# Kernel tuning notes

Hardware: AMD Instinct MI355X
Metric: run time of the kernel (lower is better)

## Reference

```python
import jax, jax.numpy as jnp
import numpy as np

B, S, D, E, H, TOPK = 4, 1024, 512, 8, 1536, 2
NORM_EPS = 1e-5

def _ln(x, w, b, eps=1e-5):
    m = jnp.mean(x, -1, keepdims=True)
    v = jnp.var(x, -1, keepdims=True)  # biased var, as torch LayerNorm
    return (x - m) * jax.lax.rsqrt(v + eps) * w + b

def _modulate(x, shift, scale):
    return x * (1 + scale[:, None, :]) + shift[:, None, :]

def setup_inputs() -> dict:
    key = jax.random.key(0)
    ks = jax.random.split(key, 14)
    s = 0.02
    return dict(
        x=jax.random.normal(ks[0], (B, S, D), jnp.float32),
        c=jax.random.normal(ks[1], (B, D), jnp.float32),
        W_ada=jax.random.normal(ks[2], (D, 6 * D), jnp.float32) * s,
        b_ada=jax.random.normal(ks[3], (6 * D,), jnp.float32) * 0.1,
        Wq=jax.random.normal(ks[4], (D, D), jnp.float32) * s,
        Wk=jax.random.normal(ks[5], (D, D), jnp.float32) * s,
        Wv=jax.random.normal(ks[6], (D, D), jnp.float32) * s,
        Wo=jax.random.normal(ks[7], (D, D), jnp.float32) * s,
        qn_w=jnp.ones((D,), jnp.float32), qn_b=jnp.zeros((D,), jnp.float32),
        kn_w=jnp.ones((D,), jnp.float32), kn_b=jnp.zeros((D,), jnp.float32),
        an_w=jnp.ones((D,), jnp.float32), an_b=jnp.zeros((D,), jnp.float32),
        fn_w=jnp.ones((D,), jnp.float32), fn_b=jnp.zeros((D,), jnp.float32),
        Wr=jax.random.normal(ks[8], (D, E), jnp.float32) * s,
        br=jnp.zeros((E,), jnp.float32),
        W1=jax.random.normal(ks[9], (E, D, H), jnp.float32) * s,
        W2=jax.random.normal(ks[10], (E, H, D), jnp.float32) * s,
        W3=jax.random.normal(ks[11], (E, D, H), jnp.float32) * s,
    )

def reference(x, c, W_ada, b_ada, Wq, Wk, Wv, Wo, qn_w, qn_b, kn_w, kn_b,
              an_w, an_b, fn_w, fn_b, Wr, br, W1, W2, W3):
    # adaLN conditioning: SiLU -> Linear -> 6 chunks
    mods = jax.nn.silu(c) @ W_ada + b_ada          # (B, 6D)
    sh_msa, sc_msa, g_msa, sh_mlp, sc_mlp, g_mlp = jnp.split(mods, 6, axis=1)

    # Attention (source attends over the FEATURE dim: scores are (B, D, D))
    h = _modulate(_ln(x, an_w, an_b, NORM_EPS), sh_msa, sc_msa)
    q = _ln(h @ Wq, qn_w, qn_b)
    k = _ln(h @ Wk, kn_w, kn_b)
    v = h @ Wv
    scores = jnp.einsum('bsd,bse->bde', q, k)      # (B, D, D), no 1/sqrt scale (as source)
    A = jax.nn.softmax(scores, axis=-1)
    attn = jnp.einsum('bde,bse->bsd', A, v) @ Wo   # (B, S, D)
    x = x + g_msa[:, None, :] * attn

    # MoE feed-forward (top-2 routing; output REPLACES x, no residual/gate per source)
    xm = _modulate(_ln(x, fn_w, fn_b, NORM_EPS), sh_mlp, sc_mlp)
    logits = xm @ Wr + br                          # (B, S, E)
    # F.normalize default dim=1 -> L2 normalize over the SEQUENCE axis (faithful)
    nrm = jnp.sqrt(jnp.sum(logits * logits, axis=1, keepdims=True))
    logits = logits / jnp.maximum(nrm, 1e-12)
    probs = jax.nn.softmax(logits, axis=-1)        # (B, S, E)
    vals, idx = jax.lax.top_k(probs, TOPK)

    T = B * S
    xf = xm.reshape(T, D)
    # dense combine weights: zero for unselected experts (same math as gather/scatter-add)
    wden = jnp.zeros((T, E), xf.dtype).at[jnp.arange(T)[:, None], idx.reshape(T, TOPK)].set(vals.reshape(T, TOPK))
    h1 = jnp.einsum('td,edh->teh', xf, W1)
    h3 = jnp.einsum('td,edh->teh', xf, W3)
    y = jnp.einsum('teh,ehd->ted', jnp.sin(h1) * h3, W2)  # sin-gated FFN per expert
    moe = jnp.einsum('ted,te->td', y, wden).reshape(B, S, D)

    avg = probs.mean(axis=0)                       # mean over batch dim only (faithful): (S, E)
    aux = jnp.sum((1.0 / E - avg) ** 2)
    return moe, aux
```

## Files before the change

kernel.cpp:

```cpp
#include <hip/hip_runtime.h>
#include <math.h>

#define NB 4
#define NS 1024
#define ND 512
#define NE 8
#define NH 1536
#define NT 4096
#define D6 3072

typedef _Float16 half_t;
typedef _Float16 f16x8 __attribute__((ext_vector_type(8)));
typedef _Float16 f16x4 __attribute__((ext_vector_type(4)));
typedef float    f32x4 __attribute__((ext_vector_type(4)));

#define LDC 136
#define TM_MAX 71

__device__ __forceinline__ void gld16(const void* g, void* l) {
  __builtin_amdgcn_global_load_lds((const __attribute__((address_space(1))) char*)g,
                                   (__attribute__((address_space(3))) char*)l, 16, 0, 0);
}

__device__ __forceinline__ int xcd_chunk(int bid, int nwg) {
  int xcd = bid & 7, ixc = bid >> 3;
  int q = nwg >> 3, r = nwg & 7;
  return (xcd < r ? xcd * (q + 1) : r * (q + 1) + (xcd - r) * q) + ixc;
}

__device__ __forceinline__ int resolve_tile(const int* __restrict__ offs, int t,
                                            int& e_out, int& m0_out) {
  int acc = 0, found = 0, ee = 0, mm = 0;
  #pragma unroll
  for (int q = 0; q < NE; ++q) {
    int ne_q = offs[q + 1] - offs[q];
    int te = (ne_q + 127) >> 7;
    if (!found && t < acc + te) { ee = q; mm = (t - acc) << 7; found = 1; }
    acc += te;
  }
  e_out = ee; m0_out = mm;
  return found;
}

__global__ __launch_bounds__(256) void k_ada(const float* __restrict__ c,
    const float* __restrict__ Wada, const float* __restrict__ bada,
    float* __restrict__ mods)
{
  __shared__ float sc[ND];
  __shared__ float part[256];
  int tid = threadIdx.x;
  int blk = blockIdx.x;
  int o0 = blk * 64;
  int b = o0 / D6;
  int j0 = o0 - b * D6;
  for (int d = tid; d < ND; d += 256) {
    float v = c[b * ND + d];
    sc[d] = v / (1.f + expf(-v));
  }
  __syncthreads();
  int j = j0 + (tid & 63);
  int kc = tid >> 6;
  float acc = 0.f;
  #pragma unroll 8
  for (int d = kc * 128; d < kc * 128 + 128; ++d)
    acc += sc[d] * Wada[(size_t)d * D6 + j];
  part[tid] = acc;
  __syncthreads();
  if (tid < 64) {
    float r = part[tid] + part[tid + 64] + part[tid + 128] + part[tid + 192]
            + bada[j0 + tid];
    mods[b * D6 + j0 + tid] = r;
  }
}

__global__ __launch_bounds__(256) void k_lnmod(const float* X, int xstride,
    float* Yf, half_t* Yh, half_t* Yl, int ystride,
    const float* __restrict__ w, const float* __restrict__ b,
    const float* __restrict__ mods, int sh_off, int sc_off,
    const float* __restrict__ Wr, const float* __restrict__ br,
    float* __restrict__ logits)
{
  __shared__ float red[16];
  __shared__ float red2[32];
  int tid = threadIdx.x;
  int row = blockIdx.x;
  int batch = row >> 10;
  const float* xr = X + (size_t)row * xstride;
  float x0 = xr[tid], x1 = xr[tid + 256];
  float s = x0 + x1, q = x0 * x0 + x1 * x1;
  #pragma unroll
  for (int off = 32; off > 0; off >>= 1) { s += __shfl_down(s, off, 64); q += __shfl_down(q, off, 64); }
  if ((tid & 63) == 0) { red[tid >> 6] = s; red[8 + (tid >> 6)] = q; }
  __syncthreads();
  if (tid == 0) {
    float S = red[0] + red[1] + red[2] + red[3];
    float Q = red[8] + red[9] + red[10] + red[11];
    float mean = S * (1.f / (float)ND);
    float var = Q * (1.f / (float)ND) - mean * mean;
    red[0] = mean; red[1] = rsqrtf(var + 1e-5f);
  }
  __syncthreads();
  float mean = red[0], rstd = red[1];
  int d0 = tid, d1 = tid + 256;
  float y0 = (x0 - mean) * rstd * w[d0] + b[d0];
  float y1 = (x1 - mean) * rstd * w[d1] + b[d1];
  if (mods) {
    const float* mb = mods + batch * D6;
    y0 = y0 * (1.f + mb[sc_off + d0]) + mb[sh_off + d0];
    y1 = y1 * (1.f + mb[sc_off + d1]) + mb[sh_off + d1];
  }
  size_t o0 = (size_t)row * ystride + d0, o1 = (size_t)row * ystride + d1;
  if (Yf) { Yf[o0] = y0; Yf[o1] = y1; }
  if (Yh) {
    half_t h0 = (half_t)y0, h1 = (half_t)y1;
    Yh[o0] = h0; Yh[o1] = h1;
    if (Yl) { Yl[o0] = (half_t)(y0 - (float)h0); Yl[o1] = (half_t)(y1 - (float)h1); }
  }
  if (Wr) {
    float p[8];
    float4 wa = *(const float4*)(Wr + d0 * 8);
    float4 wb = *(const float4*)(Wr + d0 * 8 + 4);
    float4 wc = *(const float4*)(Wr + d1 * 8);
    float4 wd = *(const float4*)(Wr + d1 * 8 + 4);
    p[0] = y0 * wa.x + y1 * wc.x; p[1] = y0 * wa.y + y1 * wc.y;
    p[2] = y0 * wa.z + y1 * wc.z; p[3] = y0 * wa.w + y1 * wc.w;
    p[4] = y0 * wb.x + y1 * wd.x; p[5] = y0 * wb.y + y1 * wd.y;
    p[6] = y0 * wb.z + y1 * wd.z; p[7] = y0 * wb.w + y1 * wd.w;
    #pragma unroll
    for (int off = 32; off > 0; off >>= 1)
      #pragma unroll
      for (int e = 0; e < 8; ++e) p[e] += __shfl_down(p[e], off, 64);
    if ((tid & 63) == 0) {
      #pragma unroll
      for (int e = 0; e < 8; ++e) red2[(tid >> 6) * 8 + e] = p[e];
    }
    __syncthreads();
    if (tid < 8)
      logits[(size_t)row * 8 + tid] = red2[tid] + red2[8 + tid] + red2[16 + tid]
                                    + red2[24 + tid] + br[tid];
  }
}

__global__ __launch_bounds__(256) void k_lnqk(float* QKV,
    const float* __restrict__ qw, const float* __restrict__ qb,
    const float* __restrict__ kw, const float* __restrict__ kb)
{
  __shared__ float red[16];
  int tid = threadIdx.x;
  int row = blockIdx.x >> 1;
  int h = blockIdx.x & 1;
  const float* w = h ? kw : qw;
  const float* b = h ? kb : qb;
  float* xr = QKV + (size_t)row * 1536 + h * 512;
  float x0 = xr[tid], x1 = xr[tid + 256];
  float s = x0 + x1, q = x0 * x0 + x1 * x1;
  #pragma unroll
  for (int off = 32; off > 0; off >>= 1) { s += __shfl_down(s, off, 64); q += __shfl_down(q, off, 64); }
  if ((tid & 63) == 0) { red[tid >> 6] = s; red[8 + (tid >> 6)] = q; }
  __syncthreads();
  if (tid == 0) {
    float S = red[0] + red[1] + red[2] + red[3];
    float Q = red[8] + red[9] + red[10] + red[11];
    float mean = S * (1.f / (float)ND);
    float var = Q * (1.f / (float)ND) - mean * mean;
    red[0] = mean; red[1] = rsqrtf(var + 1e-5f);
  }
  __syncthreads();
  float mean = red[0], rstd = red[1];
  xr[tid]       = (x0 - mean) * rstd * w[tid] + b[tid];
  xr[tid + 256] = (x1 - mean) * rstd * w[tid + 256] + b[tid + 256];
}

__global__ __launch_bounds__(256) void k_tsplit2(const float* __restrict__ QKV,
    half_t* __restrict__ H0, half_t* __restrict__ L0)
{
  __shared__ float tile[32][33];
  int z = blockIdx.z;
  half_t* outH = H0 + (size_t)z * 4194304;
  half_t* outL = L0 + (size_t)z * 4194304;
  int col0 = z * 512;
  int s0 = blockIdx.x * 32, c0 = blockIdx.y * 32;
  int tid = threadIdx.x;
  int r = tid >> 5, c = tid & 31;
  #pragma unroll
  for (int p = 0; p < 4; ++p)
    tile[r + p * 8][c] = QKV[(size_t)(s0 + r + p * 8) * 1536 + col0 + c0 + c];
  __syncthreads();
  #pragma unroll
  for (int p = 0; p < 4; ++p) {
    float v = tile[c][r + p * 8];
    half_t h = (half_t)v;
    size_t o = (size_t)(c0 + r + p * 8) * NT + s0 + c;
    outH[o] = h; outL[o] = (half_t)(v - (float)h);
  }
}

__global__ __launch_bounds__(256) void k_wsplit4(const float* __restrict__ Wq,
    const float* __restrict__ Wk, const float* __restrict__ Wv,
    const float* __restrict__ Wo, half_t* __restrict__ outH, half_t* __restrict__ outL)
{
  __shared__ float tile[32][33];
  int z = blockIdx.z;
  const float* W = (z == 0) ? Wq : (z == 1) ? Wk : (z == 2) ? Wv : Wo;
  int rowoff = z * 512;
  int k0 = blockIdx.x * 32, n0 = blockIdx.y * 32;
  int tid = threadIdx.x;
  int r = tid >> 5, c = tid & 31;
  #pragma unroll
  for (int p = 0; p < 4; ++p)
    tile[r + p * 8][c] = W[(size_t)(k0 + r + p * 8) * ND + n0 + c];
  __syncthreads();
  #pragma unroll
  for (int p = 0; p < 4; ++p) {
    float v = tile[c][r + p * 8];
    half_t h = (half_t)v;
    size_t o = (size_t)(rowoff + n0 + r + p * 8) * ND + k0 + c;
    outH[o] = h; outL[o] = (half_t)(v - (float)h);
  }
}

__global__ __launch_bounds__(256) void k_vsplit(const float* __restrict__ QKV,
    half_t* __restrict__ Vh, half_t* __restrict__ Vl)
{
  int i = blockIdx.x * 256 + threadIdx.x;
  int s = i >> 7, c = (i & 127) * 4;
  float4 v = *(const float4*)(QKV + (size_t)s * 1536 + 1024 + c);
  f16x4 h, l;
  h[0] = (half_t)v.x; l[0] = (half_t)(v.x - (float)h[0]);
  h[1] = (half_t)v.y; l[1] = (half_t)(v.y - (float)h[1]);
  h[2] = (half_t)v.z; l[2] = (half_t)(v.z - (float)h[2]);
  h[3] = (half_t)v.w; l[3] = (half_t)(v.w - (float)h[3]);
  *(f16x4*)(Vh + (size_t)s * ND + c) = h;
  *(f16x4*)(Vl + (size_t)s * ND + c) = l;
}

template<int MODE>
__global__ __launch_bounds__(256, 2) void k_gemm_hl(
    const half_t* __restrict__ Ah, const half_t* __restrict__ Al, long long sAz,
    const half_t* __restrict__ Bh, const half_t* __restrict__ Bl, long long sBz,
    int lda, int ldb, int K,
    float* __restrict__ Cf, half_t* __restrict__ Ch, half_t* __restrict__ Cl,
    long long sCz, int ldc,
    const float* __restrict__ xres, const float* __restrict__ mods)
{
  int z = blockIdx.z;
  int m0 = blockIdx.x * 128, n0 = blockIdx.y * 128;
  __shared__ __align__(16) char smem[65536];
  half_t* Sh = (half_t*)smem;
  int tid = threadIdx.x;
  int lane = tid & 63, w = tid >> 6;
  int wm = (w >> 1) * 64, wn = (w & 1) * 64;
  int qd = lane >> 4, md = lane & 15;
  int rA0 = tid >> 2;
  int sw = (((tid & 3) ^ ((tid >> 3) & 3)) << 3);

  const half_t* pAh0 = Ah + z * sAz + (size_t)(m0 + rA0) * lda + sw;
  const half_t* pAh1 = pAh0 + (size_t)64 * lda;
  const half_t* pAl0 = Al + z * sAz + (size_t)(m0 + rA0) * lda + sw;
  const half_t* pAl1 = pAl0 + (size_t)64 * lda;
  const half_t* pBh0 = Bh + z * sBz + (size_t)(n0 + rA0) * ldb + sw;
  const half_t* pBh1 = pBh0 + (size_t)64 * ldb;
  const half_t* pBl0 = Bl + z * sBz + (size_t)(n0 + rA0) * ldb + sw;
  const half_t* pBl1 = pBl0 + (size_t)64 * ldb;

  char* dAh = smem + w * 1024;
  char* dAl = smem + 16384 + w * 1024;
  char* dBh = smem + 32768 + w * 1024;
  char* dBl = smem + 49152 + w * 1024;

  f32x4 acc[4][4];
  #pragma unroll
  for (int i = 0; i < 4; ++i)
    #pragma unroll
    for (int j = 0; j < 4; ++j)
      #pragma unroll
      for (int p = 0; p < 4; ++p) acc[i][j][p] = 0.f;

  int swq  = ((qd ^ ((md >> 1) & 3)) << 3);
  int aoff = (wm + md) * 32 + swq;
  int boff = (wn + md) * 32 + swq;

#define GEMM_STAGE(p, kk) do { int kb_ = (kk); int pb_ = (p) * 8192;         \
    gld16(pAh0 + kb_, dAh + pb_); gld16(pAh1 + kb_, dAh + pb_ + 4096);       \
    gld16(pAl0 + kb_, dAl + pb_); gld16(pAl1 + kb_, dAl + pb_ + 4096);       \
    gld16(pBh0 + kb_, dBh + pb_); gld16(pBh1 + kb_, dBh + pb_ + 4096);       \
    gld16(pBl0 + kb_, dBl + pb_); gld16(pBl1 + kb_, dBl + pb_ + 4096); } while (0)

  int iters = K >> 5;
  GEMM_STAGE(0, 0);
  int cur = 0;
  #pragma unroll 1
  for (int it = 0; it < iters; ++it) {
    if (it + 1 < iters) {
      GEMM_STAGE(cur ^ 1, (it + 1) * 32);
      asm volatile("s_waitcnt vmcnt(8)\ns_barrier" ::: "memory");
    } else {
      asm volatile("s_waitcnt vmcnt(0)\ns_barrier" ::: "memory");
    }
    const half_t* Ash = Sh + cur * 4096;
    const half_t* Asl = Sh + 8192  + cur * 4096;
    const half_t* Bsh = Sh + 16384 + cur * 4096;
    const half_t* Bsl = Sh + 24576 + cur * 4096;
    f16x8 ah[4], al[4], bh[4], bl[4];
    #pragma unroll
    for (int i = 0; i < 4; ++i) {
      ah[i] = *(const f16x8*)(Ash + aoff + i * 512);
      al[i] = *(const f16x8*)(Asl + aoff + i * 512);
    }
    #pragma unroll
    for (int j = 0; j < 4; ++j) {
      bh[j] = *(const f16x8*)(Bsh + boff + j * 512);
      bl[j] = *(const f16x8*)(Bsl + boff + j * 512);
    }
    __builtin_amdgcn_s_setprio(1);
    #pragma unroll
    for (int i = 0; i < 4; ++i)
      #pragma unroll
      for (int j = 0; j < 4; ++j) {
        acc[i][j] = __builtin_amdgcn_mfma_f32_16x16x32_f16(ah[i], bh[j], acc[i][j], 0, 0, 0);
        acc[i][j] = __builtin_amdgcn_mfma_f32_16x16x32_f16(ah[i], bl[j], acc[i][j], 0, 0, 0);
        acc[i][j] = __builtin_amdgcn_mfma_f32_16x16x32_f16(al[i], bh[j], acc[i][j], 0, 0, 0);
      }
    __builtin_amdgcn_s_setprio(0);
    asm volatile("s_barrier" ::: "memory");
    cur ^= 1;
  }
#undef GEMM_STAGE

  if (MODE == 1) {
    half_t* Cs = (half_t*)smem;
    __syncthreads();
    #pragma unroll
    for (int i = 0; i < 4; ++i)
      #pragma unroll
      for (int j = 0; j < 4; ++j)
        #pragma unroll
        for (int p = 0; p < 4; ++p)
          Cs[(wm + 16 * i + qd * 4 + p) * LDC + wn + 16 * j + md] = (half_t)acc[i][j][p];
    __syncthreads();
    #pragma unroll
    for (int it2 = 0; it2 < 8; ++it2) {
      int chunk = it2 * 256 + tid;
      int r = chunk >> 4, c8 = (chunk & 15) * 8;
      *(f16x8*)(Ch + z * sCz + (size_t)(m0 + r) * ldc + n0 + c8) = *(const f16x8*)(Cs + r * LDC + c8);
    }
    __syncthreads();
    #pragma unroll
    for (int i = 0; i < 4; ++i)
      #pragma unroll
      for (int j = 0; j < 4; ++j)
        #pragma unroll
        for (int p = 0; p < 4; ++p) {
          float v = acc[i][j][p];
          half_t h = (half_t)v;
          Cs[(wm + 16 * i + qd * 4 + p) * LDC + wn + 16 * j + md] = (half_t)(v - (float)h);
        }
    __syncthreads();
    #pragma unroll
    for (int it2 = 0; it2 < 8; ++it2) {
      int chunk = it2 * 256 + tid;
      int r = chunk >> 4, c8 = (chunk & 15) * 8;
      *(f16x8*)(Cl + z * sCz + (size_t)(m0 + r) * ldc + n0 + c8) = *(const f16x8*)(Cs + r * LDC + c8);
    }
  } else {
    #pragma unroll
    for (int i = 0; i < 4; ++i)
      #pragma unroll
      for (int p = 0; p < 4; ++p) {
        int r = m0 + wm + 16 * i + qd * 4 + p;
        float* cp = Cf + z * sCz + (size_t)r * ldc + n0 + wn + md;
        if (MODE == 2) {
          int batch = r >> 10;
          const float* mb = mods + batch * D6 + 2 * ND;
          const float* xp = xres + (size_t)r * ldc + n0 + wn + md;
          #pragma unroll
          for (int j = 0; j < 4; ++j) {
            int col = wn + md + 16 * j;
            cp[16 * j] = xp[16 * j] + mb[n0 + col] * acc[i][j][p];
          }
        } else {
          #pragma unroll
          for (int j = 0; j < 4; ++j) cp[16 * j] = acc[i][j][p];
        }
      }
  }
}

__global__ __launch_bounds__(256) void k_softmax512_sum4(const float* __restrict__ SC4,
    half_t* __restrict__ Ph, half_t* __restrict__ Pl)
{
  __shared__ float red[16];
  int tid = threadIdx.x;
  int row = blockIdx.x;
  int b = row >> 9, d = row & 511;
  const float* r0 = SC4 + ((size_t)(b * 4 + 0) << 18) + (size_t)d * ND;
  const float* r1 = SC4 + ((size_t)(b * 4 + 1) << 18) + (size_t)d * ND;
  const float* r2 = SC4 + ((size_t)(b * 4 + 2) << 18) + (size_t)d * ND;
  const float* r3 = SC4 + ((size_t)(b * 4 + 3) << 18) + (size_t)d * ND;
  float x0 = r0[tid] + r1[tid] + r2[tid] + r3[tid];
  float x1 = r0[tid + 256] + r1[tid + 256] + r2[tid + 256] + r3[tid + 256];
  float m = fmaxf(x0, x1);
  #pragma unroll
  for (int off = 32; off > 0; off >>= 1) m = fmaxf(m, __shfl_down(m, off, 64));
  if ((tid & 63) == 0) red[tid >> 6] = m;
  __syncthreads();
  if (tid == 0) red[0] = fmaxf(fmaxf(red[0], red[1]), fmaxf(red[2], red[3]));
  __syncthreads();
  m = red[0];
  float e0 = expf(x0 - m), e1 = expf(x1 - m);
  float s = e0 + e1;
  #pragma unroll
  for (int off = 32; off > 0; off >>= 1) s += __shfl_down(s, off, 64);
  if ((tid & 63) == 0) red[8 + (tid >> 6)] = s;
  __syncthreads();
  if (tid == 0) red[8] = red[8] + red[9] + red[10] + red[11];
  __syncthreads();
  float inv = 1.f / red[8];
  float p0 = e0 * inv, p1 = e1 * inv;
  size_t base = (size_t)row * ND;
  half_t h0 = (half_t)p0, h1 = (half_t)p1;
  Ph[base + tid] = h0;       Pl[base + tid] = (half_t)(p0 - (float)h0);
  Ph[base + tid + 256] = h1; Pl[base + tid + 256] = (half_t)(p1 - (float)h1);
}

__global__ __launch_bounds__(256) void k_colnorm(const float* __restrict__ logits,
    float* __restrict__ nrm)
{
  __shared__ float red[8];
  int tid = threadIdx.x;
  int b = blockIdx.x >> 3, e = blockIdx.x & 7;
  float acc = 0.f;
  for (int s = tid; s < NS; s += 256) {
    float l = logits[((size_t)(b << 10) + s) * NE + e];
    acc += l * l;
  }
  #pragma unroll
  for (int off = 32; off > 0; off >>= 1) acc += __shfl_down(acc, off, 64);
  if ((tid & 63) == 0) red[tid >> 6] = acc;
  __syncthreads();
  if (tid == 0) nrm[b * NE + e] = sqrtf(red[0] + red[1] + red[2] + red[3]);
}

__global__ __launch_bounds__(1024) void k_route(const float* __restrict__ logits,
    const float* __restrict__ nrm, float* __restrict__ probs,
    float* __restrict__ wsel, int* __restrict__ offs_g,
    int* __restrict__ list, int* __restrict__ inv)
{
  __shared__ unsigned char sisel[8192];
  __shared__ int cw[8][16][8];
  __shared__ int soffs[9];
  __shared__ float snrm[32];
  int tid = threadIdx.x;
  int lane = tid & 63, wv = tid >> 6;
  if (tid < 32) snrm[tid] = fmaxf(nrm[tid], 1e-12f);
  __syncthreads();
  #pragma unroll 1
  for (int c = 0; c < 4; ++c) {
    int t = c * 1024 + tid;
    int b = t >> 10;
    float p[8];
    float4 l0 = *(const float4*)(logits + (size_t)t * 8);
    float4 l1 = *(const float4*)(logits + (size_t)t * 8 + 4);
    p[0] = l0.x / snrm[b * 8 + 0]; p[1] = l0.y / snrm[b * 8 + 1];
    p[2] = l0.z / snrm[b * 8 + 2]; p[3] = l0.w / snrm[b * 8 + 3];
    p[4] = l1.x / snrm[b * 8 + 4]; p[5] = l1.y / snrm[b * 8 + 5];
    p[6] = l1.z / snrm[b * 8 + 6]; p[7] = l1.w / snrm[b * 8 + 7];
    float mx = p[0];
    #pragma unroll
    for (int e = 1; e < 8; ++e) mx = fmaxf(mx, p[e]);
    float s = 0.f;
    #pragma unroll
    for (int e = 0; e < 8; ++e) { p[e] = expf(p[e] - mx); s += p[e]; }
    float invs = 1.f / s;
    #pragma unroll
    for (int e = 0; e < 8; ++e) { p[e] *= invs; probs[(size_t)t * 8 + e] = p[e]; }
    int i1 = 0;
    #pragma unroll
    for (int e = 1; e < 8; ++e) if (p[e] > p[i1]) i1 = e;
    int i2 = (i1 == 0) ? 1 : 0;
    #pragma unroll
    for (int e = 0; e < 8; ++e) if (e != i1 && p[e] > p[i2]) i2 = e;
    wsel[t * 2] = p[i1]; wsel[t * 2 + 1] = p[i2];
    sisel[t * 2] = (unsigned char)i1; sisel[t * 2 + 1] = (unsigned char)i2;
  }
  __syncthreads();
  #pragma unroll 1
  for (int c = 0; c < 8; ++c) {
    int em = sisel[c * 1024 + tid];
    #pragma unroll
    for (int e = 0; e < 8; ++e) {
      unsigned long long mask = __ballot(em == e);
      if (lane == 0) cw[c][wv][e] = (int)__popcll(mask);
    }
  }
  __syncthreads();
  if (tid < 8) {
    int e = tid, run = 0;
    for (int c = 0; c < 8; ++c)
      for (int w2 = 0; w2 < 16; ++w2) { int v = cw[c][w2][e]; cw[c][w2][e] = run; run += v; }
    soffs[e] = run;
  }
  __syncthreads();
  if (tid == 0) {
    int a = 0;
    #pragma unroll
    for (int e = 0; e < 8; ++e) { int v = soffs[e]; soffs[e] = a; a += v; }
    soffs[8] = a;
  }
  __syncthreads();
  if (tid < 9) offs_g[tid] = soffs[tid];
  #pragma unroll 1
  for (int c = 0; c < 8; ++c) {
    int idx = c * 1024 + tid;
    int em = sisel[idx];
    int rk = 0;
    #pragma unroll
    for (int e = 0; e < 8; ++e) {
      unsigned long long mask = __ballot(em == e);
      if (em == e) rk = (int)__popcll(mask & ((1ull << lane) - 1ull));
    }
    int slot = soffs[em] + cw[c][wv][em] + rk;
    list[slot] = idx >> 1;
    inv[idx] = slot;
  }
}

__global__ __launch_bounds__(256) void k_aux(const float* __restrict__ probs,
    float* __restrict__ outAux)
{
  __shared__ float red[8];
  int tid = threadIdx.x;
  float acc = 0.f;
  for (int s = tid; s < NS; s += 256) {
    #pragma unroll
    for (int e = 0; e < NE; ++e) {
      float a = probs[(size_t)s * NE + e] + probs[(size_t)(NS + s) * NE + e]
              + probs[(size_t)(2 * NS + s) * NE + e] + probs[(size_t)(3 * NS + s) * NE + e];
      float d = 0.125f - a * 0.25f;
      acc += d * d;
    }
  }
  #pragma unroll
  for (int off = 32; off > 0; off >>= 1) acc += __shfl_down(acc, off, 64);
  if ((tid & 63) == 0) red[tid >> 6] = acc;
  __syncthreads();
  if (tid == 0) *outAux = red[0] + red[1] + red[2] + red[3];
}

__global__ __launch_bounds__(256) void k_tcast13(const float* __restrict__ W1,
    const float* __restrict__ W3, half_t* __restrict__ W1t, half_t* __restrict__ W3t)
{
  __shared__ float tile[32][33];
  int z = blockIdx.z;
  int sel = z >> 3, e = z & 7;
  const float* We = (sel ? W3 : W1) + (size_t)e * ND * NH;
  half_t* Wte = (sel ? W3t : W1t) + (size_t)e * ND * NH;
  int k0 = blockIdx.x * 32, n0 = blockIdx.y * 32;
  int tid = threadIdx.x;
  int r = tid >> 5, c = tid & 31;
  #pragma unroll
  for (int p = 0; p < 4; ++p)
    tile[r + p * 8][c] = We[(size_t)(k0 + r + p * 8) * NH + n0 + c];
  __syncthreads();
  #pragma unroll
  for (int p = 0; p < 4; ++p)
    Wte[(size_t)(n0 + r + p * 8) * ND + k0 + c] = (half_t)tile[c][r + p * 8];
}

__global__ __launch_bounds__(256) void k_tcastW2(const float* __restrict__ W,
    half_t* __restrict__ Wt)
{
  __shared__ float tile[32][33];
  const float* We = W + (size_t)blockIdx.z * NH * ND;
  half_t* Wte = Wt + (size_t)blockIdx.z * NH * ND;
  int k0 = blockIdx.x * 32, n0 = blockIdx.y * 32;
  int tid = threadIdx.x;
  int r = tid >> 5, c = tid & 31;
  #pragma unroll
  for (int p = 0; p < 4; ++p)
    tile[r + p * 8][c] = We[(size_t)(k0 + r + p * 8) * ND + n0 + c];
  __syncthreads();
  #pragma unroll
  for (int p = 0; p < 4; ++p)
    Wte[(size_t)(n0 + r + p * 8) * NH + k0 + c] = (half_t)tile[c][r + p * 8];
}

__global__ __launch_bounds__(256, 3) void k_ffn_fused(const half_t* __restrict__ xmh,
    const half_t* __restrict__ W1t, const half_t* __restrict__ W3t,
    const int* __restrict__ list, const int* __restrict__ offs,
    half_t* __restrict__ gate)
{
  int bx = xcd_chunk(blockIdx.x, TM_MAX * 12);
  int n0 = (bx % 12) * 128;
  int t  = bx / 12;
  int e, m0;
  if (!resolve_tile(offs, t, e, m0)) return;
  int base = offs[e], ne = offs[e + 1] - base;

  __shared__ __align__(16) char smem[49664];
  half_t* Sh = (half_t*)smem;
  int* rowt = (int*)(smem + 49152);
  int tid = threadIdx.x;
  if (tid < 128) {
    int rr = m0 + tid;
    rowt[tid] = (rr < ne) ? list[base + rr] : 0;
  }
  __syncthreads();

  int lane = tid & 63, w = tid >> 6;
  int wm = (w >> 1) * 64, wn = (w & 1) * 64;
  int qd = lane >> 4, md = lane & 15;
  int rA0 = tid >> 2;
  int sw = (((tid & 3) ^ ((tid >> 3) & 3)) << 3);
  int tok0 = rowt[rA0], tok1 = rowt[rA0 + 64];

  const half_t* gA0  = xmh + (size_t)tok0 * ND + sw;
  const half_t* gA1  = xmh + (size_t)tok1 * ND + sw;
  const half_t* gB10 = W1t + ((size_t)e * NH + n0 + rA0) * ND + sw;
  const half_t* gB11 = gB10 + (size_t)64 * ND;
  const half_t* gB30 = W3t + ((size_t)e * NH + n0 + rA0) * ND + sw;
  const half_t* gB31 = gB30 + (size_t)64 * ND;

  char* dA  = smem + w * 1024;
  char* dB1 = smem + 16384 + w * 1024;
  char* dB3 = smem + 32768 + w * 1024;

  f32x4 acc1[4][4], acc3[4][4];
  #pragma unroll
  for (int i = 0; i < 4; ++i)
    #pragma unroll
    for (int j = 0; j < 4; ++j)
      #pragma unroll
      for (int p = 0; p < 4; ++p) { acc1[i][j][p] = 0.f; acc3[i][j][p] = 0.f; }

  int swq  = ((qd ^ ((md >> 1) & 3)) << 3);
  int aoff = (wm + md) * 32 + swq;
  int boff = (wn + md) * 32 + swq;

#define FFN_STAGE(p, kk) do { int kb_ = (kk); int pb_ = (p) * 8192;          \
    gld16(gA0  + kb_, dA  + pb_); gld16(gA1  + kb_, dA  + pb_ + 4096);       \
    gld16(gB10 + kb_, dB1 + pb_); gld16(gB11 + kb_, dB1 + pb_ + 4096);       \
    gld16(gB30 + kb_, dB3 + pb_); gld16(gB31 + kb_, dB3 + pb_ + 4096); } while (0)

  FFN_STAGE(0, 0);
  int cur = 0;
  #pragma unroll 1
  for (int it = 0; it < 16; ++it) {
    if (it + 1 < 16) {
      FFN_STAGE(cur ^ 1, (it + 1) * 32);
      asm volatile("s_waitcnt vmcnt(6)\ns_barrier" ::: "memory");
    } else {
      asm volatile("s_waitcnt vmcnt(0)\ns_barrier" ::: "memory");
    }
    const half_t* As  = Sh + cur * 4096;
    const half_t* B1s = Sh + 8192  + cur * 4096;
    const half_t* B3s = Sh + 16384 + cur * 4096;
    f16x8 a[4];
    #pragma unroll
    for (int i = 0; i < 4; ++i) a[i] = *(const f16x8*)(As + aoff + i * 512);
    __builtin_amdgcn_s_setprio(1);
    #pragma unroll
    for (int j = 0; j < 4; ++j) {
      f16x8 b1 = *(const f16x8*)(B1s + boff + j * 512);
      f16x8 b3 = *(const f16x8*)(B3s + boff + j * 512);
      #pragma unroll
      for (int i = 0; i < 4; ++i) {
        acc1[i][j] = __builtin_amdgcn_mfma_f32_16x16x32_f16(a[i], b1, acc1[i][j], 0, 0, 0);
        acc3[i][j] = __builtin_amdgcn_mfma_f32_16x16x32_f16(a[i], b3, acc3[i][j], 0, 0, 0);
      }
    }
    __builtin_amdgcn_s_setprio(0);
    asm volatile("s_barrier" ::: "memory");
    cur ^= 1;
  }
#undef FFN_STAGE

  half_t* Cs = (half_t*)smem;
  #pragma unroll
  for (int i = 0; i < 4; ++i)
    #pragma unroll
    for (int j = 0; j < 4; ++j)
      #pragma unroll
      for (int p = 0; p < 4; ++p) {
        int rr = wm + 16 * i + qd * 4 + p;
        int cc = wn + 16 * j + md;
        Cs[rr * LDC + cc] = (half_t)(__sinf(acc1[i][j][p]) * acc3[i][j][p]);
      }
  __syncthreads();
  #pragma unroll
  for (int it = 0; it < 8; ++it) {
    int chunk = it * 256 + tid;
    int rr = chunk >> 4, c8 = (chunk & 15) * 8;
    if (m0 + rr < ne) {
      *(f16x8*)(gate + (size_t)(base + m0 + rr) * NH + n0 + c8) = *(const f16x8*)(Cs + rr * LDC + c8);
    }
  }
}

__global__ __launch_bounds__(256, 4) void k_moe2_mfma(const half_t* __restrict__ gate,
    const half_t* __restrict__ W2t, const int* __restrict__ offs,
    float* __restrict__ P)
{
  int bx = xcd_chunk(blockIdx.x, TM_MAX * 4);
  int n0 = (bx & 3) * 128;
  int t = bx >> 2;
  int e, m0;
  if (!resolve_tile(offs, t, e, m0)) return;
  int base = offs[e], ne = offs[e + 1] - base;

  __shared__ __align__(16) char smem[32768];
  half_t* Sh = (half_t*)smem;
  int tid = threadIdx.x;
  int lane = tid & 63, w = tid >> 6;
  int wm = (w >> 1) * 64, wn = (w & 1) * 64;
  int qd = lane >> 4, md = lane & 15;
  int rA0 = tid >> 2;
  int sw = (((tid & 3) ^ ((tid >> 3) & 3)) << 3);

  int ar0 = m0 + rA0;      if (ar0 >= ne) ar0 = ne - 1;
  int ar1 = m0 + rA0 + 64; if (ar1 >= ne) ar1 = ne - 1;
  const half_t* gA0 = gate + (size_t)(base + ar0) * NH + sw;
  const half_t* gA1 = gate + (size_t)(base + ar1) * NH + sw;
  const half_t* gB0 = W2t + ((size_t)e * ND + n0 + rA0) * NH + sw;
  const half_t* gB1 = gB0 + (size_t)64 * NH;

  char* dA = smem + w * 1024;
  char* dB = smem + 16384 + w * 1024;

  f32x4 acc[4][4];
  #pragma unroll
  for (int i = 0; i < 4; ++i)
    #pragma unroll
    for (int j = 0; j < 4; ++j)
      #pragma unroll
      for (int p = 0; p < 4; ++p) acc[i][j][p] = 0.f;

  int swq  = ((qd ^ ((md >> 1) & 3)) << 3);
  int aoff = (wm + md) * 32 + swq;
  int boff = (wn + md) * 32 + swq;

#define MOE2_STAGE(p, kk) do { int kb_ = (kk); int pb_ = (p) * 8192;         \
    gld16(gA0 + kb_, dA + pb_); gld16(gA1 + kb_, dA + pb_ + 4096);           \
    gld16(gB0 + kb_, dB + pb_); gld16(gB1 + kb_, dB + pb_ + 4096); } while (0)

  MOE2_STAGE(0, 0);
  int cur = 0;
  #pragma unroll 1
  for (int it = 0; it < 48; ++it) {
    if (it + 1 < 48) {
      MOE2_STAGE(cur ^ 1, (it + 1) * 32);
      asm volatile("s_waitcnt vmcnt(4)\ns_barrier" ::: "memory");
    } else {
      asm volatile("s_waitcnt vmcnt(0)\ns_barrier" ::: "memory");
    }
    const half_t* As = Sh + cur * 4096;
    const half_t* Bs = Sh + 8192 + cur * 4096;
    f16x8 a[4], b[4];
    #pragma unroll
    for (int i = 0; i < 4; ++i) a[i] = *(const f16x8*)(As + aoff + i * 512);
    #pragma unroll
    for (int j = 0; j < 4; ++j) b[j] = *(const f16x8*)(Bs + boff + j * 512);
    __builtin_amdgcn_s_setprio(1);
    #pragma unroll
    for (int j = 0; j < 4; ++j)
      #pragma unroll
      for (int i = 0; i < 4; ++i)
        acc[i][j] = __builtin_amdgcn_mfma_f32_16x16x32_f16(a[i], b[j], acc[i][j], 0, 0, 0);
    __builtin_amdgcn_s_setprio(0);
    asm volatile("s_barrier" ::: "memory");
    cur ^= 1;
  }
#undef MOE2_STAGE

  #pragma unroll
  for (int i = 0; i < 4; ++i)
    #pragma unroll
    for (int p = 0; p < 4; ++p) {
      int gr = m0 + wm + 16 * i + qd * 4 + p;
      if (gr < ne) {
        float* pp = P + (size_t)(base + gr) * ND + n0 + wn + md;
        #pragma unroll
        for (int j = 0; j < 4; ++j)
          pp[16 * j] = acc[i][j][p];
      }
    }
}

__global__ __launch_bounds__(256) void k_moe_reduce(const float* __restrict__ P,
    const int* __restrict__ inv, const float* __restrict__ wsel,
    float* __restrict__ out)
{
  int i = blockIdx.x * 256 + threadIdx.x;
  int t = i >> 7, d4 = i & 127;
  int s1 = inv[t * 2], s2 = inv[t * 2 + 1];
  float w1 = wsel[t * 2], w2 = wsel[t * 2 + 1];
  const float4* P4 = (const float4*)P;
  float4 a = P4[(size_t)s1 * 128 + d4];
  float4 b = P4[(size_t)s2 * 128 + d4];
  float4 o;
  o.x = w1 * a.x + w2 * b.x;
  o.y = w1 * a.y + w2 * b.y;
  o.z = w1 * a.z + w2 * b.z;
  o.w = w1 * a.w + w2 * b.w;
  ((float4*)out)[i] = o;
}

static const size_t BO_MODS  = 0;
static const size_t BO_HH    = 65536;
static const size_t BO_HL2   = 4259840;
static const size_t BO_PH    = 4259840;
static const size_t BO_PL    = 6357056;
static const size_t BO_WALLH = 8454144;
static const size_t BO_WALLL = 10551296;
static const size_t BO_QKV   = 12648448;
static const size_t BO_A0H   = 12648448;
static const size_t BO_A0L   = 16842752;
static const size_t BO_SC4   = 21037056;
static const size_t BO_X2    = 21037056;
static const size_t BO_XM    = 29425664;
static const size_t BO_QTH   = 37814272;
static const size_t BO_QTL   = 42008576;
static const size_t BO_KTH   = 46202880;
static const size_t BO_KTL   = 50397184;
static const size_t BO_VH    = 54591488;
static const size_t BO_VL    = 58785792;
static const size_t BO_W1T   = 37814272;
static const size_t BO_XMH   = 50397184;
static const size_t BO_W3T   = 65536;
static const size_t BO_GATE  = 12648448;
static const size_t BO_W2T   = 65536;
static const size_t BO_P     = 37814272;
static const size_t BO_LOGI  = 62980096;
static const size_t BO_NRM   = 63111168;
static const size_t BO_PROB  = 63111296;
static const size_t BO_WSEL  = 63242368;
static const size_t BO_INTS  = 63307904;

extern "C" void kernel_launch(void* const* d_in, const int* in_sizes, int n_in,
                              void* d_out, int out_size, void* d_ws, size_t ws_size,
                              hipStream_t stream)
{
  const float* x    = (const float*)d_in[0];
  const float* c    = (const float*)d_in[1];
  const float* Wada = (const float*)d_in[2];
  const float* bada = (const float*)d_in[3];
  const float* Wq   = (const float*)d_in[4];
  const float* Wk   = (const float*)d_in[5];
  const float* Wv   = (const float*)d_in[6];
  const float* Wo   = (const float*)d_in[7];
  const float* qn_w = (const float*)d_in[8];
  const float* qn_b = (const float*)d_in[9];
  const float* kn_w = (const float*)d_in[10];
  const float* kn_b = (const float*)d_in[11];
  const float* an_w = (const float*)d_in[12];
  const float* an_b = (const float*)d_in[13];
  const float* fn_w = (const float*)d_in[14];
  const float* fn_b = (const float*)d_in[15];
  const float* Wr   = (const float*)d_in[16];
  const float* br   = (const float*)d_in[17];
  const float* W1   = (const float*)d_in[18];
  const float* W2   = (const float*)d_in[19];
  const float* W3   = (const float*)d_in[20];
  float* out = (float*)d_out;
  char*  ws8 = (char*)d_ws;
  float* MODS = (float*)(ws8 + BO_MODS);
  half_t* Hh = (half_t*)(ws8 + BO_HH),   *Hl = (half_t*)(ws8 + BO_HL2);
  half_t* Ph = (half_t*)(ws8 + BO_PH),   *Pl = (half_t*)(ws8 + BO_PL);
  half_t* WALLH = (half_t*)(ws8 + BO_WALLH), *WALLL = (half_t*)(ws8 + BO_WALLL);
  half_t* WoTh = WALLH + (size_t)1536 * ND,  *WoTl = WALLL + (size_t)1536 * ND;
  float* QKV = (float*)(ws8 + BO_QKV);
  half_t* A0h = (half_t*)(ws8 + BO_A0H), *A0l = (half_t*)(ws8 + BO_A0L);
  float* SC4 = (float*)(ws8 + BO_SC4);
  float* X2  = (float*)(ws8 + BO_X2);
  float* XM  = (float*)(ws8 + BO_XM);
  half_t* qTh = (half_t*)(ws8 + BO_QTH), *qTl = (half_t*)(ws8 + BO_QTL);
  half_t* kTh = (half_t*)(ws8 + BO_KTH), *kTl = (half_t*)(ws8 + BO_KTL);
  half_t* Vh  = (half_t*)(ws8 + BO_VH),  *Vl  = (half_t*)(ws8 + BO_VL);
  half_t* W1T = (half_t*)(ws8 + BO_W1T);
  half_t* W3T = (half_t*)(ws8 + BO_W3T);
  half_t* W2T = (half_t*)(ws8 + BO_W2T);
  half_t* XMH = (half_t*)(ws8 + BO_XMH);
  half_t* GATEH = (half_t*)(ws8 + BO_GATE);
  float* PBUF = (float*)(ws8 + BO_P);
  float* LOGI = (float*)(ws8 + BO_LOGI);
  float* NRM  = (float*)(ws8 + BO_NRM);
  float* PROB = (float*)(ws8 + BO_PROB);
  float* WSEL = (float*)(ws8 + BO_WSEL);
  int* ib   = (int*)(ws8 + BO_INTS);
  int* offs = ib + 8208;
  int* list = ib + 8224;
  int* inv  = ib + 16416;

  k_ada<<<192, 256, 0, stream>>>(c, Wada, bada, MODS);
  k_wsplit4<<<dim3(16, 16, 4), 256, 0, stream>>>(Wq, Wk, Wv, Wo, WALLH, WALLL);
  k_lnmod<<<NT, 256, 0, stream>>>(x, ND, nullptr, Hh, Hl, ND, an_w, an_b, MODS, 0, 512,
                                  nullptr, nullptr, nullptr);
  k_gemm_hl<0><<<dim3(32, 12, 1), 256, 0, stream>>>(Hh, Hl, 0, WALLH, WALLL, 0,
      ND, ND, ND, QKV, nullptr, nullptr, 0, 1536, nullptr, nullptr);
  k_lnqk<<<2 * NT, 256, 0, stream>>>(QKV, qn_w, qn_b, kn_w, kn_b);
  k_tsplit2<<<dim3(128, 16, 2), 256, 0, stream>>>(QKV, qTh, qTl);
  k_vsplit<<<2048, 256, 0, stream>>>(QKV, Vh, Vl);
  k_gemm_hl<0><<<dim3(4, 4, 16), 256, 0, stream>>>(qTh, qTl, 256, kTh, kTl, 256,
      NT, NT, 256, SC4, nullptr, nullptr, 262144, ND, nullptr, nullptr);
  k_softmax512_sum4<<<2048, 256, 0, stream>>>(SC4, Ph, Pl);
  k_gemm_hl<1><<<dim3(8, 4, 4), 256, 0, stream>>>(Vh, Vl, 524288, Ph, Pl, 262144,
      ND, ND, ND, nullptr, A0h, A0l, 524288, ND, nullptr, nullptr);
  k_gemm_hl<2><<<dim3(32, 4, 1), 256, 0, stream>>>(A0h, A0l, 0, WoTh, WoTl, 0,
      ND, ND, ND, X2, nullptr, nullptr, 0, ND, x, MODS);
  k_lnmod<<<NT, 256, 0, stream>>>(X2, ND, XM, XMH, nullptr, ND, fn_w, fn_b, MODS, 1536, 2048,
                                  Wr, br, LOGI);
  k_colnorm<<<32, 256, 0, stream>>>(LOGI, NRM);
  k_route<<<1, 1024, 0, stream>>>(LOGI, NRM, PROB, WSEL, offs, list, inv);
  k_aux<<<1, 256, 0, stream>>>(PROB, out + (size_t)NT * ND);
  k_tcast13<<<dim3(16, 48, 16), 256, 0, stream>>>(W1, W3, W1T, W3T);
  k_ffn_fused<<<TM_MAX * 12, 256, 0, stream>>>(XMH, W1T, W3T, list, offs, GATEH);
  k_tcastW2<<<dim3(48, 16, 8), 256, 0, stream>>>(W2, W2T);
  k_moe2_mfma<<<TM_MAX * 4, 256, 0, stream>>>(GATEH, W2T, offs, PBUF);
  k_moe_reduce<<<2048, 256, 0, stream>>>(PBUF, inv, WSEL, out);
}
```

Before: 396.3 us.

## Fuse V hi/lo split into QKV GEMM epilogue and widen weight transposes

Adds a GEMM epilogue mode that writes the V columns of the QKV projection straight out as fp16 hi/lo pairs, which removes the separate k_vsplit kernel and its extra read of QKV. The weight transpose-cast kernels now use 64x64 tiles with float4 loads and f16x4 stores instead of 32x32 scalar accesses, aiming for better memory-transaction efficiency. k_ada is split into twice as many blocks with shorter reductions to spread the adaLN matvec over more CUs. In exchange, the V epilogue uses scattered scalar half stores, and the QKV buffer's V columns are no longer written, which relies on nothing else reading them.

```diff
diff --git a/kernel.cpp b/kernel.cpp
--- a/kernel.cpp
+++ b/kernel.cpp
@@ -50,7 +50,7 @@
   __shared__ float part[256];
   int tid = threadIdx.x;
   int blk = blockIdx.x;
-  int o0 = blk * 64;
+  int o0 = blk * 32;
   int b = o0 / D6;
   int j0 = o0 - b * D6;
   for (int d = tid; d < ND; d += 256) {
@@ -58,17 +58,18 @@
     sc[d] = v / (1.f + expf(-v));
   }
   __syncthreads();
-  int j = j0 + (tid & 63);
-  int kc = tid >> 6;
+  int j = j0 + (tid & 31);
+  int kc = tid >> 5;
   float acc = 0.f;
   #pragma unroll 8
-  for (int d = kc * 128; d < kc * 128 + 128; ++d)
+  for (int d = kc * 64; d < kc * 64 + 64; ++d)
     acc += sc[d] * Wada[(size_t)d * D6 + j];
   part[tid] = acc;
   __syncthreads();
-  if (tid < 64) {
-    float r = part[tid] + part[tid + 64] + part[tid + 128] + part[tid + 192]
-            + bada[j0 + tid];
+  if (tid < 32) {
+    float r = bada[j0 + tid];
+    #pragma unroll
+    for (int k = 0; k < 8; ++k) r += part[tid + 32 * k];
     mods[b * D6 + j0 + tid] = r;
   }
 }
@@ -219,21 +220,6 @@
   }
 }
 
-__global__ __launch_bounds__(256) void k_vsplit(const float* __restrict__ QKV,
-    half_t* __restrict__ Vh, half_t* __restrict__ Vl)
-{
-  int i = blockIdx.x * 256 + threadIdx.x;
-  int s = i >> 7, c = (i & 127) * 4;
-  float4 v = *(const float4*)(QKV + (size_t)s * 1536 + 1024 + c);
-  f16x4 h, l;
-  h[0] = (half_t)v.x; l[0] = (half_t)(v.x - (float)h[0]);
-  h[1] = (half_t)v.y; l[1] = (half_t)(v.y - (float)h[1]);
-  h[2] = (half_t)v.z; l[2] = (half_t)(v.z - (float)h[2]);
-  h[3] = (half_t)v.w; l[3] = (half_t)(v.w - (float)h[3]);
-  *(f16x4*)(Vh + (size_t)s * ND + c) = h;
-  *(f16x4*)(Vl + (size_t)s * ND + c) = l;
-}
-
 template<int MODE>
 __global__ __launch_bounds__(256, 2) void k_gemm_hl(
     const half_t* __restrict__ Ah, const half_t* __restrict__ Al, long long sAz,
@@ -241,7 +227,8 @@
     int lda, int ldb, int K,
     float* __restrict__ Cf, half_t* __restrict__ Ch, half_t* __restrict__ Cl,
     long long sCz, int ldc,
-    const float* __restrict__ xres, const float* __restrict__ mods)
+    const float* __restrict__ xres, const float* __restrict__ mods,
+    half_t* __restrict__ vh, half_t* __restrict__ vl)
 {
   int z = blockIdx.z;
   int m0 = blockIdx.x * 128, n0 = blockIdx.y * 128;
@@ -362,6 +349,23 @@
       int r = chunk >> 4, c8 = (chunk & 15) * 8;
       *(f16x8*)(Cl + z * sCz + (size_t)(m0 + r) * ldc + n0 + c8) = *(const f16x8*)(Cs + r * LDC + c8);
     }
+  } else if (MODE == 3 && n0 >= 1024) {
+    #pragma unroll
+    for (int i = 0; i < 4; ++i)
+      #pragma unroll
+      for (int p = 0; p < 4; ++p) {
+        int r = m0 + wm + 16 * i + qd * 4 + p;
+        int vc = n0 - 1024 + wn + md;
+        half_t* hp = vh + (size_t)r * ND + vc;
+        half_t* lp = vl + (size_t)r * ND + vc;
+        #pragma unroll
+        for (int j = 0; j < 4; ++j) {
+          float v = acc[i][j][p];
+          half_t h = (half_t)v;
+          hp[16 * j] = h;
+          lp[16 * j] = (half_t)(v - (float)h);
+        }
+      }
   } else {
     #pragma unroll
     for (int i = 0; i < 4; ++i)
@@ -550,39 +554,57 @@
 __global__ __launch_bounds__(256) void k_tcast13(const float* __restrict__ W1,
     const float* __restrict__ W3, half_t* __restrict__ W1t, half_t* __restrict__ W3t)
 {
-  __shared__ float tile[32][33];
+  __shared__ float tile[64][68];
   int z = blockIdx.z;
   int sel = z >> 3, e = z & 7;
   const float* We = (sel ? W3 : W1) + (size_t)e * ND * NH;
   half_t* Wte = (sel ? W3t : W1t) + (size_t)e * ND * NH;
-  int k0 = blockIdx.x * 32, n0 = blockIdx.y * 32;
-  int tid = threadIdx.x;
-  int r = tid >> 5, c = tid & 31;
-  #pragma unroll
-  for (int p = 0; p < 4; ++p)
-    tile[r + p * 8][c] = We[(size_t)(k0 + r + p * 8) * NH + n0 + c];
-  __syncthreads();
-  #pragma unroll
-  for (int p = 0; p < 4; ++p)
-    Wte[(size_t)(n0 + r + p * 8) * ND + k0 + c] = (half_t)tile[c][r + p * 8];
+  int k0 = blockIdx.x * 64, n0 = blockIdx.y * 64;
+  int tid = threadIdx.x;
+  int r = tid >> 4, c4 = tid & 15;
+  #pragma unroll
+  for (int p = 0; p < 4; ++p) {
+    int row = r + p * 16;
+    float4 v = *(const float4*)(We + (size_t)(k0 + row) * NH + n0 + c4 * 4);
+    tile[row][c4 * 4 + 0] = v.x; tile[row][c4 * 4 + 1] = v.y;
+    tile[row][c4 * 4 + 2] = v.z; tile[row][c4 * 4 + 3] = v.w;
+  }
+  __syncthreads();
+  #pragma unroll
+  for (int p = 0; p < 4; ++p) {
+    int orow = r + p * 16;
+    f16x4 h;
+    #pragma unroll
+    for (int i = 0; i < 4; ++i) h[i] = (half_t)tile[c4 * 4 + i][orow];
+    *(f16x4*)(Wte + (size_t)(n0 + orow) * ND + k0 + c4 * 4) = h;
+  }
 }
 
 __global__ __launch_bounds__(256) void k_tcastW2(const float* __restrict__ W,
     half_t* __restrict__ Wt)
 {
-  __shared__ float tile[32][33];
+  __shared__ float tile[64][68];
   const float* We = W + (size_t)blockIdx.z * NH * ND;
   half_t* Wte = Wt + (size_t)blockIdx.z * NH * ND;
-  int k0 = blockIdx.x * 32, n0 = blockIdx.y * 32;
-  int tid = threadIdx.x;
-  int r = tid >> 5, c = tid & 31;
-  #pragma unroll
-  for (int p = 0; p < 4; ++p)
-    tile[r + p * 8][c] = We[(size_t)(k0 + r + p * 8) * ND + n0 + c];
-  __syncthreads();
-  #pragma unroll
-  for (int p = 0; p < 4; ++p)
-    Wte[(size_t)(n0 + r + p * 8) * NH + k0 + c] = (half_t)tile[c][r + p * 8];
+  int k0 = blockIdx.x * 64, n0 = blockIdx.y * 64;
+  int tid = threadIdx.x;
+  int r = tid >> 4, c4 = tid & 15;
+  #pragma unroll
+  for (int p = 0; p < 4; ++p) {
+    int row = r + p * 16;
+    float4 v = *(const float4*)(We + (size_t)(k0 + row) * ND + n0 + c4 * 4);
+    tile[row][c4 * 4 + 0] = v.x; tile[row][c4 * 4 + 1] = v.y;
+    tile[row][c4 * 4 + 2] = v.z; tile[row][c4 * 4 + 3] = v.w;
+  }
+  __syncthreads();
+  #pragma unroll
+  for (int p = 0; p < 4; ++p) {
+    int orow = r + p * 16;
+    f16x4 h;
+    #pragma unroll
+    for (int i = 0; i < 4; ++i) h[i] = (half_t)tile[c4 * 4 + i][orow];
+    *(f16x4*)(Wte + (size_t)(n0 + orow) * NH + k0 + c4 * 4) = h;
+  }
 }
 
 __global__ __launch_bounds__(256, 3) void k_ffn_fused(const half_t* __restrict__ xmh,
@@ -891,30 +913,29 @@
   int* list = ib + 8224;
   int* inv  = ib + 16416;
 
-  k_ada<<<192, 256, 0, stream>>>(c, Wada, bada, MODS);
+  k_ada<<<384, 256, 0, stream>>>(c, Wada, bada, MODS);
   k_wsplit4<<<dim3(16, 16, 4), 256, 0, stream>>>(Wq, Wk, Wv, Wo, WALLH, WALLL);
   k_lnmod<<<NT, 256, 0, stream>>>(x, ND, nullptr, Hh, Hl, ND, an_w, an_b, MODS, 0, 512,
                                   nullptr, nullptr, nullptr);
-  k_gemm_hl<0><<<dim3(32, 12, 1), 256, 0, stream>>>(Hh, Hl, 0, WALLH, WALLL, 0,
-      ND, ND, ND, QKV, nullptr, nullptr, 0, 1536, nullptr, nullptr);
+  k_gemm_hl<3><<<dim3(32, 12, 1), 256, 0, stream>>>(Hh, Hl, 0, WALLH, WALLL, 0,
+      ND, ND, ND, QKV, nullptr, nullptr, 0, 1536, nullptr, nullptr, Vh, Vl);
   k_lnqk<<<2 * NT, 256, 0, stream>>>(QKV, qn_w, qn_b, kn_w, kn_b);
   k_tsplit2<<<dim3(128, 16, 2), 256, 0, stream>>>(QKV, qTh, qTl);
-  k_vsplit<<<2048, 256, 0, stream>>>(QKV, Vh, Vl);
   k_gemm_hl<0><<<dim3(4, 4, 16), 256, 0, stream>>>(qTh, qTl, 256, kTh, kTl, 256,
-      NT, NT, 256, SC4, nullptr, nullptr, 262144, ND, nullptr, nullptr);
+      NT, NT, 256, SC4, nullptr, nullptr, 262144, ND, nullptr, nullptr, nullptr, nullptr);
   k_softmax512_sum4<<<2048, 256, 0, stream>>>(SC4, Ph, Pl);
   k_gemm_hl<1><<<dim3(8, 4, 4), 256, 0, stream>>>(Vh, Vl, 524288, Ph, Pl, 262144,
-      ND, ND, ND, nullptr, A0h, A0l, 524288, ND, nullptr, nullptr);
+      ND, ND, ND, nullptr, A0h, A0l, 524288, ND, nullptr, nullptr, nullptr, nullptr);
   k_gemm_hl<2><<<dim3(32, 4, 1), 256, 0, stream>>>(A0h, A0l, 0, WoTh, WoTl, 0,
-      ND, ND, ND, X2, nullptr, nullptr, 0, ND, x, MODS);
+      ND, ND, ND, X2, nullptr, nullptr, 0, ND, x, MODS, nullptr, nullptr);
   k_lnmod<<<NT, 256, 0, stream>>>(X2, ND, XM, XMH, nullptr, ND, fn_w, fn_b, MODS, 1536, 2048,
                                   Wr, br, LOGI);
   k_colnorm<<<32, 256, 0, stream>>>(LOGI, NRM);
   k_route<<<1, 1024, 0, stream>>>(LOGI, NRM, PROB, WSEL, offs, list, inv);
   k_aux<<<1, 256, 0, stream>>>(PROB, out + (size_t)NT * ND);
-  k_tcast13<<<dim3(16, 48, 16), 256, 0, stream>>>(W1, W3, W1T, W3T);
+  k_tcast13<<<dim3(8, 24, 16), 256, 0, stream>>>(W1, W3, W1T, W3T);
   k_ffn_fused<<<TM_MAX * 12, 256, 0, stream>>>(XMH, W1T, W3T, list, offs, GATEH);
-  k_tcastW2<<<dim3(48, 16, 8), 256, 0, stream>>>(W2, W2T);
+  k_tcastW2<<<dim3(24, 8, 8), 256, 0, stream>>>(W2, W2T);
   k_moe2_mfma<<<TM_MAX * 4, 256, 0, stream>>>(GATEH, W2T, offs, PBUF);
   k_moe_reduce<<<2048, 256, 0, stream>>>(PBUF, inv, WSEL, out);
 }
```

Result: faster. 385.4 us (-2.8%).
